# Performance work log

Measured on AMD Instinct MI355X. Metric: run time of the kernel, lower is better.

Reference implementation:

```python
import jax, jax.numpy as jnp
import numpy as np

B, S, D, H = 2, 2048, 1024, 16
HD = D // H          # 64
HALF = HD // 2       # 32
EPS = 1e-6           # RMSNorm eps (module default eps=1e-6)


def setup_inputs() -> dict:
    key = jax.random.key(0)
    ks = jax.random.split(key, 6)
    x = jax.random.normal(ks[0], (B, S, D), jnp.float32)
    scale = 1.0 / np.sqrt(D)
    Wq = jax.random.normal(ks[1], (D, D), jnp.float32) * scale
    Wk = jax.random.normal(ks[2], (D, D), jnp.float32) * scale
    Wv = jax.random.normal(ks[3], (D, D), jnp.float32) * scale
    Wo = jax.random.normal(ks[4], (D, D), jnp.float32) * scale
    bq = jnp.zeros((D,), jnp.float32)
    bk = jnp.zeros((D,), jnp.float32)
    bv = jnp.zeros((D,), jnp.float32)
    bo = jnp.zeros((D,), jnp.float32)
    gq = jnp.ones((D,), jnp.float32)   # norm_q weight
    gk = jnp.ones((D,), jnp.float32)   # norm_k weight
    # Standard RoPE angles: pos * 10000^(-2i/head_dim); freqs = exp(i*ang)
    pos = jnp.arange(S, dtype=jnp.float32)
    inv_freq = 1.0 / (10000.0 ** (jnp.arange(0, HD, 2, dtype=jnp.float32) / HD))
    ang = pos[:, None] * inv_freq[None, :]          # (S, HALF)
    return dict(x=x, Wq=Wq, bq=bq, Wk=Wk, bk=bk, Wv=Wv, bv=bv, Wo=Wo, bo=bo,
                gq=gq, gk=gk, freqs_cos=jnp.cos(ang), freqs_sin=jnp.sin(ang))


def _rmsnorm(x, g):
    # x * rsqrt(mean(x^2) + eps) * g, computed in fp32 as in the torch module
    return x * jax.lax.rsqrt(jnp.mean(x * x, axis=-1, keepdims=True) + EPS) * g


def _rope(x, cos, sin):
    # x: (B,S,D) packed heads; rotate consecutive (even,odd) pairs per head.
    xr = x.reshape(B, S, H, HALF, 2)
    x0, x1 = xr[..., 0], xr[..., 1]
    c = cos[None, :, None, :]  # (1,S,1,HALF)
    s = sin[None, :, None, :]
    o0 = x0 * c - x1 * s
    o1 = x0 * s + x1 * c
    return jnp.stack([o0, o1], axis=-1).reshape(B, S, D)


def reference(x, Wq, bq, Wk, bk, Wv, bv, Wo, bo, gq, gk, freqs_cos, freqs_sin):
    q = _rmsnorm(x @ Wq.T + bq, gq)
    k = _rmsnorm(x @ Wk.T + bk, gk)
    v = x @ Wv.T + bv
    q = _rope(q, freqs_cos, freqs_sin)
    k = _rope(k, freqs_cos, freqs_sin)
    # SDPA (non-causal, as F.scaled_dot_product_attention default call)
    qh = q.reshape(B, S, H, HD)
    kh = k.reshape(B, S, H, HD)
    vh = v.reshape(B, S, H, HD)
    scores = jnp.einsum('bqhd,bkhd->bhqk', qh, kh) / np.sqrt(HD)
    attn = jax.nn.softmax(scores, axis=-1)
    out = jnp.einsum('bhqk,bkhd->bqhd', attn, vh).reshape(B, S, D)
    return out @ Wo.T + bo
```

## Files before the change

### kernel.cpp

```cpp
#include <hip/hip_runtime.h>

typedef unsigned short u16;
typedef unsigned int u32;
typedef u16 u16x4 __attribute__((ext_vector_type(4)));
typedef u16 u16x8 __attribute__((ext_vector_type(8)));
typedef u32 u32x2 __attribute__((ext_vector_type(2)));
typedef float f32x4 __attribute__((ext_vector_type(4)));
typedef __bf16 bf16x2 __attribute__((ext_vector_type(2)));
typedef __bf16 bf16x8 __attribute__((ext_vector_type(8)));

#define GLOAD16(gp, lp)                                             \
  __builtin_amdgcn_global_load_lds(                                 \
      (const __attribute__((address_space(1))) void*)(gp),          \
      (__attribute__((address_space(3))) void*)(lp), 16, 0, 0)

__device__ __forceinline__ u16 f2bf(float f) {
  unsigned int u = __builtin_bit_cast(unsigned int, f);
  u += 0x7FFFu + ((u >> 16) & 1u);
  return (u16)(u >> 16);
}
__device__ __forceinline__ float bf2f(u16 h) {
  return __builtin_bit_cast(float, (u32)h << 16);
}

__global__ __launch_bounds__(256) void f2b_kernel(const float* __restrict__ in,
                                                  u16* __restrict__ out, int n4) {
  int i = blockIdx.x * 256 + threadIdx.x;
  if (i < n4) {
    f32x4 v = *(const f32x4*)(in + (size_t)i * 4);
    u16x4 o;
    o[0] = f2bf(v[0]); o[1] = f2bf(v[1]); o[2] = f2bf(v[2]); o[3] = f2bf(v[3]);
    *(u16x4*)(out + (size_t)i * 4) = o;
  }
}

__global__ __launch_bounds__(256) void f2bw_kernel(const float* __restrict__ s0,
    const float* __restrict__ s1, const float* __restrict__ s2,
    const float* __restrict__ s3, u16* __restrict__ dst) {
  const int y = blockIdx.y;
  const float* s = (y == 0) ? s0 : ((y == 1) ? s1 : ((y == 2) ? s2 : s3));
  int i = blockIdx.x * 256 + threadIdx.x;
  f32x4 v = *(const f32x4*)(s + (size_t)i * 4);
  u16x4 o;
  o[0] = f2bf(v[0]); o[1] = f2bf(v[1]); o[2] = f2bf(v[2]); o[3] = f2bf(v[3]);
  *(u16x4*)(dst + (size_t)y * 1048576 + (size_t)i * 4) = o;
}

__device__ __forceinline__ void gemm_core(const u16* __restrict__ A,
                                          const u16* __restrict__ W,
                                          int bm0, int bn0,
                                          u16* ldsA, u16* ldsB,
                                          f32x4 acc[4][4]) {
  const int tid = threadIdx.x;
  const int l = tid & 63;
  const int lr = l & 15, lk = l >> 4;
  const int w = tid >> 6;
  const int wr = w >> 1, wc = w & 1;
  const int srow = tid >> 2, sko = (tid & 3) << 3;
  auto stage = [&](int kt, int buf) {
#pragma unroll
    for (int it = 0; it < 2; ++it) {
      int row = it * 64 + srow;
      GLOAD16(A + (size_t)(bm0 + row) * 1024 + kt * 32 + sko,
              ldsA + buf * 4096 + (it * 256 + tid) * 8);
      GLOAD16(W + (size_t)(bn0 + row) * 1024 + kt * 32 + sko,
              ldsB + buf * 4096 + (it * 256 + tid) * 8);
    }
  };
  stage(0, 0);
  __syncthreads();
  int cur = 0;
  for (int kt = 0; kt < 32; ++kt) {
    if (kt + 1 < 32) stage(kt + 1, cur ^ 1);
    const u16* lA = ldsA + cur * 4096;
    const u16* lB = ldsB + cur * 4096;
    bf16x8 af[4], bfr[4];
#pragma unroll
    for (int m = 0; m < 4; ++m)
      af[m] = *(const bf16x8*)(lA + (wr * 64 + m * 16 + lr) * 32 + lk * 8);
#pragma unroll
    for (int n = 0; n < 4; ++n)
      bfr[n] = *(const bf16x8*)(lB + (wc * 64 + n * 16 + lr) * 32 + lk * 8);
#pragma unroll
    for (int m = 0; m < 4; ++m)
#pragma unroll
      for (int n = 0; n < 4; ++n)
        acc[m][n] = __builtin_amdgcn_mfma_f32_16x16x32_bf16(af[m], bfr[n], acc[m][n], 0, 0, 0);
    __syncthreads();
    cur ^= 1;
  }
}

__global__ __launch_bounds__(256) void qkv_gemm(const u16* __restrict__ xb,
    const u16* __restrict__ wq, const u16* __restrict__ wk, const u16* __restrict__ wv,
    const float* __restrict__ bq, const float* __restrict__ bk, const float* __restrict__ bv,
    u16* __restrict__ Qb, u16* __restrict__ Kb, u16* __restrict__ Vt) {
  __shared__ u16 ldsA[2 * 4096];
  __shared__ u16 ldsB[2 * 4096];
  const int z = blockIdx.z;
  const u16* W = (z == 0) ? wq : ((z == 1) ? wk : wv);
  const float* bias = (z == 0) ? bq : ((z == 1) ? bk : bv);
  const int bm0 = blockIdx.x * 128, bn0 = blockIdx.y * 128;
  const f32x4 zf = {0.f, 0.f, 0.f, 0.f};
  f32x4 acc[4][4];
#pragma unroll
  for (int m = 0; m < 4; ++m)
#pragma unroll
    for (int n = 0; n < 4; ++n) acc[m][n] = zf;
  gemm_core(xb, W, bm0, bn0, ldsA, ldsB, acc);
  const int tid = threadIdx.x, l = tid & 63, lr = l & 15, lk = l >> 4;
  const int w = tid >> 6, wr = w >> 1, wc = w & 1;
  float bcol[4];
#pragma unroll
  for (int n = 0; n < 4; ++n) bcol[n] = bias[bn0 + wc * 64 + n * 16 + lr];
  if (z < 2) {
    u16* outp = z ? Kb : Qb;
#pragma unroll
    for (int m = 0; m < 4; ++m)
#pragma unroll
      for (int n = 0; n < 4; ++n)
#pragma unroll
        for (int r = 0; r < 4; ++r) {
          int row = bm0 + wr * 64 + m * 16 + lk * 4 + r;
          int col = bn0 + wc * 64 + n * 16 + lr;
          outp[(size_t)row * 1024 + col] = f2bf(acc[m][n][r] + bcol[n]);
        }
  } else {
#pragma unroll
    for (int m = 0; m < 4; ++m)
#pragma unroll
      for (int n = 0; n < 4; ++n) {
        int row = bm0 + wr * 64 + m * 16 + lk * 4;
        int col = bn0 + wc * 64 + n * 16 + lr;
        int b = row >> 11, s = row & 2047, hh = col >> 6, hd = col & 63;
        u16x4 o;
#pragma unroll
        for (int r = 0; r < 4; ++r) o[r] = f2bf(acc[m][n][r] + bcol[n]);
        *(u16x4*)(Vt + (((size_t)((b * 16 + hh) * 64 + hd)) << 11) + s) = o;
      }
  }
}

__global__ __launch_bounds__(256) void proj_gemm(const u16* __restrict__ ctx,
    const u16* __restrict__ wo, const float* __restrict__ bo, float* __restrict__ out) {
  __shared__ u16 ldsA[2 * 4096];
  __shared__ u16 ldsB[2 * 4096];
  const int bm0 = blockIdx.x * 128, bn0 = blockIdx.y * 128;
  const f32x4 zf = {0.f, 0.f, 0.f, 0.f};
  f32x4 acc[4][4];
#pragma unroll
  for (int m = 0; m < 4; ++m)
#pragma unroll
    for (int n = 0; n < 4; ++n) acc[m][n] = zf;
  gemm_core(ctx, wo, bm0, bn0, ldsA, ldsB, acc);
  const int tid = threadIdx.x, l = tid & 63, lr = l & 15, lk = l >> 4;
  const int w = tid >> 6, wr = w >> 1, wc = w & 1;
  float bcol[4];
#pragma unroll
  for (int n = 0; n < 4; ++n) bcol[n] = bo[bn0 + wc * 64 + n * 16 + lr];
#pragma unroll
  for (int m = 0; m < 4; ++m)
#pragma unroll
    for (int n = 0; n < 4; ++n)
#pragma unroll
      for (int r = 0; r < 4; ++r) {
        int row = bm0 + wr * 64 + m * 16 + lk * 4 + r;
        int col = bn0 + wc * 64 + n * 16 + lr;
        out[(size_t)row * 1024 + col] = acc[m][n][r] + bcol[n];
      }
}

__global__ __launch_bounds__(256) void rmsrope(const u16* __restrict__ Qb,
    const u16* __restrict__ Kb, const float* __restrict__ gq, const float* __restrict__ gk,
    const float* __restrict__ fc, const float* __restrict__ fs,
    u16* __restrict__ Qh, u16* __restrict__ Kh) {
  const int row = blockIdx.x;
  const int which = blockIdx.y;
  const u16* src = (which ? Kb : Qb) + (size_t)row * 1024;
  const float* g = which ? gk : gq;
  u16* dst = which ? Kh : Qh;
  const int t = threadIdx.x;
  u16x4 raw = *(const u16x4*)(src + t * 4);
  float v0 = bf2f(raw[0]), v1 = bf2f(raw[1]), v2 = bf2f(raw[2]), v3 = bf2f(raw[3]);
  float ss = v0 * v0 + v1 * v1 + v2 * v2 + v3 * v3;
#pragma unroll
  for (int mm = 1; mm < 64; mm <<= 1) ss += __shfl_xor(ss, mm);
  __shared__ float red[4];
  if ((t & 63) == 0) red[t >> 6] = ss;
  __syncthreads();
  float rstd = rsqrtf((red[0] + red[1] + red[2] + red[3]) * (1.0f / 1024.0f) + 1e-6f);
  if (!which) rstd *= 0.18033688011112042f;
  int d = t * 4, hh = d >> 6, dh = d & 63, p = dh >> 1;
  int s = row & 2047, b = row >> 11;
  float c0 = fc[(s << 5) + p], s0 = fs[(s << 5) + p];
  float c1 = fc[(s << 5) + p + 1], s1 = fs[(s << 5) + p + 1];
  float x0 = v0 * rstd * g[d];
  float x1 = v1 * rstd * g[d + 1];
  float x2 = v2 * rstd * g[d + 2];
  float x3 = v3 * rstd * g[d + 3];
  u16x4 o;
  o[0] = f2bf(x0 * c0 - x1 * s0);
  o[1] = f2bf(x0 * s0 + x1 * c0);
  o[2] = f2bf(x2 * c1 - x3 * s1);
  o[3] = f2bf(x2 * s1 + x3 * c1);
  *(u16x4*)(dst + ((size_t)((b << 4) + hh) * 2048 + s) * 64 + dh) = o;
}

__global__ __launch_bounds__(512, 4) void attn_kernel(const u16* __restrict__ Qh,
    const u16* __restrict__ Kh, const u16* __restrict__ Vt, u16* __restrict__ ctx) {
  __shared__ u16 Kbuf[2][4096];
  __shared__ u16 Vbuf[2][4096];
  __shared__ __attribute__((aligned(16))) u32 Pl[8][16][36];
  const int tid = threadIdx.x;
  const int w = tid >> 6, l = tid & 63, lr = l & 15, lk = l >> 4;
  const int id = blockIdx.x;
  const int qt = (id >> 3) & 15;
  const int hb = (id & 7) | ((id >> 7) << 3);
  const int h = hb & 15, b = hb >> 4;
  const int bh = b * 16 + h;
  const u16* Q = Qh + (size_t)bh * 2048 * 64;
  const u16* K = Kh + (size_t)bh * 2048 * 64;
  const u16* V = Vt + (size_t)bh * 64 * 2048;
  const int q0 = qt * 128;
  const int srow = tid >> 3;
  const int kslot = (tid & 7) ^ (srow & 7);
  bf16x8 qf[2];
#pragma unroll
  for (int kh = 0; kh < 2; ++kh)
    qf[kh] = *(const bf16x8*)(Q + (size_t)(q0 + w * 16 + lr) * 64 + kh * 32 + lk * 8);
  const f32x4 zf = {0.f, 0.f, 0.f, 0.f};
  f32x4 O[4];
  float Mrun = -1e30f, lsum = 0.f;
#pragma unroll
  for (int n = 0; n < 4; ++n) O[n] = zf;
  GLOAD16(K + ((size_t)srow << 6) + kslot * 8, &Kbuf[0][tid * 8]);
  GLOAD16(V + ((size_t)srow << 11) + kslot * 8, &Vbuf[0][tid * 8]);
  __syncthreads();
  int cur = 0;
  for (int kb = 0; kb < 32; ++kb) {
    if (kb + 1 < 32) {
      GLOAD16(K + ((size_t)((kb + 1) * 64 + srow) << 6) + kslot * 8, &Kbuf[cur ^ 1][tid * 8]);
      GLOAD16(V + ((size_t)srow << 11) + (kb + 1) * 64 + kslot * 8, &Vbuf[cur ^ 1][tid * 8]);
    }
    f32x4 sc[4];
#pragma unroll
    for (int n = 0; n < 4; ++n) sc[n] = zf;
    __builtin_amdgcn_s_setprio(1);
#pragma unroll
    for (int n = 0; n < 4; ++n)
#pragma unroll
      for (int kh = 0; kh < 2; ++kh) {
        bf16x8 kf = *(const bf16x8*)(&Kbuf[cur][(n * 16 + lr) * 64 + (((kh * 4 + lk) ^ (lr & 7)) << 3)]);
        sc[n] = __builtin_amdgcn_mfma_f32_16x16x32_bf16(kf, qf[kh], sc[n], 0, 0, 0);
      }
    __builtin_amdgcn_s_setprio(0);
    float bm = fmaxf(fmaxf(sc[0][0], sc[0][1]), fmaxf(sc[0][2], sc[0][3]));
#pragma unroll
    for (int n = 1; n < 4; ++n)
      bm = fmaxf(bm, fmaxf(fmaxf(sc[n][0], sc[n][1]), fmaxf(sc[n][2], sc[n][3])));
    bm = fmaxf(bm, __shfl_xor(bm, 16));
    bm = fmaxf(bm, __shfl_xor(bm, 32));
    if (!__all(bm <= Mrun + 1.4427f)) {
      float nM = fmaxf(Mrun, bm);
      float f = exp2f(Mrun - nM);
      lsum *= f;
#pragma unroll
      for (int n = 0; n < 4; ++n)
#pragma unroll
        for (int r = 0; r < 4; ++r) O[n][r] *= f;
      Mrun = nM;
    }
    float rs = 0.f;
#pragma unroll
    for (int n = 0; n < 4; ++n) {
      u32 pw[2];
#pragma unroll
      for (int c = 0; c < 2; ++c) {
        float p0 = exp2f(sc[n][2 * c] - Mrun);
        float p1 = exp2f(sc[n][2 * c + 1] - Mrun);
        rs += p0 + p1;
        bf16x2 pp;
        pp[0] = (__bf16)p0; pp[1] = (__bf16)p1;
        pw[c] = __builtin_bit_cast(u32, pp);
      }
      u32x2 pv = {pw[0], pw[1]};
      *(u32x2*)&Pl[w][lr][8 * n + 2 * lk] = pv;
    }
    rs += __shfl_xor(rs, 16);
    rs += __shfl_xor(rs, 32);
    lsum += rs;
    __builtin_amdgcn_s_setprio(1);
#pragma unroll
    for (int kk = 0; kk < 2; ++kk) {
      bf16x8 pa = *(const bf16x8*)&Pl[w][lr][16 * kk + 4 * lk];
#pragma unroll
      for (int n = 0; n < 4; ++n) {
        bf16x8 vb = *(const bf16x8*)(&Vbuf[cur][(n * 16 + lr) * 64 + (((kk * 4 + lk) ^ (lr & 7)) << 3)]);
        O[n] = __builtin_amdgcn_mfma_f32_16x16x32_bf16(vb, pa, O[n], 0, 0, 0);
      }
    }
    __builtin_amdgcn_s_setprio(0);
    __syncthreads();
    cur ^= 1;
  }
  float inv = 1.0f / lsum;
  const size_t rowbase = ((size_t)((b << 11) + q0 + w * 16 + lr)) * 1024 + (h << 6);
#pragma unroll
  for (int n = 0; n < 4; ++n) {
    u16x4 o4;
#pragma unroll
    for (int r = 0; r < 4; ++r) o4[r] = f2bf(O[n][r] * inv);
    *(u16x4*)(ctx + rowbase + n * 16 + 4 * lk) = o4;
  }
}

extern "C" void kernel_launch(void* const* d_in, const int* in_sizes, int n_in,
                              void* d_out, int out_size, void* d_ws, size_t ws_size,
                              hipStream_t stream) {
  (void)in_sizes; (void)n_in; (void)out_size; (void)ws_size;
  const float* x  = (const float*)d_in[0];
  const float* Wq = (const float*)d_in[1];
  const float* bq = (const float*)d_in[2];
  const float* Wk = (const float*)d_in[3];
  const float* bk = (const float*)d_in[4];
  const float* Wv = (const float*)d_in[5];
  const float* bv = (const float*)d_in[6];
  const float* Wo = (const float*)d_in[7];
  const float* bo = (const float*)d_in[8];
  const float* gq = (const float*)d_in[9];
  const float* gk = (const float*)d_in[10];
  const float* fc = (const float*)d_in[11];
  const float* fs = (const float*)d_in[12];
  float* out = (float*)d_out;
  char* ws = (char*)d_ws;
  u16*  xb  = (u16*)(ws + 0);
  u16*  wqb = (u16*)(ws + 8388608);
  u16*  wkb = (u16*)(ws + 10485760);
  u16*  wvb = (u16*)(ws + 12582912);
  u16*  wob = (u16*)(ws + 14680064);
  u16*  Qfb = (u16*)(ws + 16777216);
  u16*  Kfb = (u16*)(ws + 25165824);
  u16*  Qhb = (u16*)(ws + 33554432);
  u16*  Khb = (u16*)(ws + 41943040);
  u16*  Vtb = (u16*)(ws + 50331648);
  u16*  ctx = (u16*)(ws + 58720256);

  f2b_kernel<<<4096, 256, 0, stream>>>(x, xb, 1048576);
  f2bw_kernel<<<dim3(1024, 4), 256, 0, stream>>>(Wq, Wk, Wv, Wo, wqb);
  qkv_gemm<<<dim3(32, 8, 3), 256, 0, stream>>>(xb, wqb, wkb, wvb, bq, bk, bv, Qfb, Kfb, Vtb);
  rmsrope<<<dim3(4096, 2), 256, 0, stream>>>(Qfb, Kfb, gq, gk, fc, fs, Qhb, Khb);
  attn_kernel<<<512, 512, 0, stream>>>(Qhb, Khb, Vtb, ctx);
  proj_gemm<<<dim3(32, 8), 256, 0, stream>>>(ctx, wob, bo, out);
}
```

Measured before the change: 157.7 us.

## Triple-buffer LDS tiles with prefetch distance two in GEMM and attention

```diff
diff --git a/kernel.cpp b/kernel.cpp
--- a/kernel.cpp
+++ b/kernel.cpp
@@ -68,10 +68,14 @@
     }
   };
   stage(0, 0);
-  __syncthreads();
-  int cur = 0;
+  stage(1, 1);
+  int cur = 0, nx2 = 2;
   for (int kt = 0; kt < 32; ++kt) {
-    if (kt + 1 < 32) stage(kt + 1, cur ^ 1);
+    if (kt < 31) asm volatile("s_waitcnt vmcnt(4)" ::: "memory");
+    else         asm volatile("s_waitcnt vmcnt(0)" ::: "memory");
+    __builtin_amdgcn_s_barrier();
+    __builtin_amdgcn_sched_barrier(0);
+    if (kt + 2 < 32) stage(kt + 2, nx2);
     const u16* lA = ldsA + cur * 4096;
     const u16* lB = ldsB + cur * 4096;
     bf16x8 af[4], bfr[4];
@@ -86,8 +90,8 @@
 #pragma unroll
       for (int n = 0; n < 4; ++n)
         acc[m][n] = __builtin_amdgcn_mfma_f32_16x16x32_bf16(af[m], bfr[n], acc[m][n], 0, 0, 0);
-    __syncthreads();
-    cur ^= 1;
+    cur = (cur == 2) ? 0 : cur + 1;
+    nx2 = (nx2 == 2) ? 0 : nx2 + 1;
   }
 }
 
@@ -95,8 +99,8 @@
     const u16* __restrict__ wq, const u16* __restrict__ wk, const u16* __restrict__ wv,
     const float* __restrict__ bq, const float* __restrict__ bk, const float* __restrict__ bv,
     u16* __restrict__ Qb, u16* __restrict__ Kb, u16* __restrict__ Vt) {
-  __shared__ u16 ldsA[2 * 4096];
-  __shared__ u16 ldsB[2 * 4096];
+  __shared__ u16 ldsA[3 * 4096];
+  __shared__ u16 ldsB[3 * 4096];
   const int z = blockIdx.z;
   const u16* W = (z == 0) ? wq : ((z == 1) ? wk : wv);
   const float* bias = (z == 0) ? bq : ((z == 1) ? bk : bv);
@@ -143,8 +147,8 @@
 
 __global__ __launch_bounds__(256) void proj_gemm(const u16* __restrict__ ctx,
     const u16* __restrict__ wo, const float* __restrict__ bo, float* __restrict__ out) {
-  __shared__ u16 ldsA[2 * 4096];
-  __shared__ u16 ldsB[2 * 4096];
+  __shared__ u16 ldsA[3 * 4096];
+  __shared__ u16 ldsB[3 * 4096];
   const int bm0 = blockIdx.x * 128, bn0 = blockIdx.y * 128;
   const f32x4 zf = {0.f, 0.f, 0.f, 0.f};
   f32x4 acc[4][4];
@@ -208,8 +212,8 @@
 
 __global__ __launch_bounds__(512, 4) void attn_kernel(const u16* __restrict__ Qh,
     const u16* __restrict__ Kh, const u16* __restrict__ Vt, u16* __restrict__ ctx) {
-  __shared__ u16 Kbuf[2][4096];
-  __shared__ u16 Vbuf[2][4096];
+  __shared__ u16 Kbuf[3][4096];
+  __shared__ u16 Vbuf[3][4096];
   __shared__ __attribute__((aligned(16))) u32 Pl[8][16][36];
   const int tid = threadIdx.x;
   const int w = tid >> 6, l = tid & 63, lr = l & 15, lk = l >> 4;
@@ -235,12 +239,17 @@
   for (int n = 0; n < 4; ++n) O[n] = zf;
   GLOAD16(K + ((size_t)srow << 6) + kslot * 8, &Kbuf[0][tid * 8]);
   GLOAD16(V + ((size_t)srow << 11) + kslot * 8, &Vbuf[0][tid * 8]);
-  __syncthreads();
-  int cur = 0;
+  GLOAD16(K + ((size_t)(64 + srow) << 6) + kslot * 8, &Kbuf[1][tid * 8]);
+  GLOAD16(V + ((size_t)srow << 11) + 64 + kslot * 8, &Vbuf[1][tid * 8]);
+  int cur = 0, nx2 = 2;
   for (int kb = 0; kb < 32; ++kb) {
-    if (kb + 1 < 32) {
-      GLOAD16(K + ((size_t)((kb + 1) * 64 + srow) << 6) + kslot * 8, &Kbuf[cur ^ 1][tid * 8]);
-      GLOAD16(V + ((size_t)srow << 11) + (kb + 1) * 64 + kslot * 8, &Vbuf[cur ^ 1][tid * 8]);
+    if (kb < 31) asm volatile("s_waitcnt vmcnt(2)" ::: "memory");
+    else         asm volatile("s_waitcnt vmcnt(0)" ::: "memory");
+    __builtin_amdgcn_s_barrier();
+    __builtin_amdgcn_sched_barrier(0);
+    if (kb + 2 < 32) {
+      GLOAD16(K + ((size_t)((kb + 2) * 64 + srow) << 6) + kslot * 8, &Kbuf[nx2][tid * 8]);
+      GLOAD16(V + ((size_t)srow << 11) + (kb + 2) * 64 + kslot * 8, &Vbuf[nx2][tid * 8]);
     }
     f32x4 sc[4];
 #pragma unroll
@@ -300,8 +309,8 @@
       }
     }
     __builtin_amdgcn_s_setprio(0);
-    __syncthreads();
-    cur ^= 1;
+    cur = (cur == 2) ? 0 : cur + 1;
+    nx2 = (nx2 == 2) ? 0 : nx2 + 1;
   }
   float inv = 1.0f / lsum;
   const size_t rowbase = ((size_t)((b << 11) + q0 + w * 16 + lr)) * 1024 + (h << 6);
```

New measurement: 148.0 us. 6.2% less time.
